# Kernel optimization log

Measured on AMD Instinct MI355X. Metric: run time of the kernel, lower is better.

The kernel has to match this reference:

```python
import jax, jax.numpy as jnp
import numpy as np

PS = 32
D = 256


def setup_inputs() -> dict:
    key = jax.random.key(0)
    ks = jax.random.split(key, 9)
    B, L = 32, 32768
    s_in = 1.0 / np.sqrt(PS)
    s_d = 1.0 / np.sqrt(D)
    return {
        "x": jax.random.normal(ks[0], (B, L), dtype=jnp.float32),
        "W_proj": jax.random.normal(ks[1], (PS, D), dtype=jnp.float32) * s_in,
        "b_proj": jnp.zeros((D,), jnp.float32),
        "W_qkv": jax.random.normal(ks[2], (D, 3 * D), dtype=jnp.float32) * s_d,
        "b_qkv": jnp.zeros((3 * D,), jnp.float32),
        "W_out": jax.random.normal(ks[3], (D, D), dtype=jnp.float32) * s_d,
        "b_out": jnp.zeros((D,), jnp.float32),
        "W_head": jax.random.normal(ks[4], (D, PS), dtype=jnp.float32) * s_d,
        "b_head": jnp.zeros((PS,), jnp.float32),
    }


def reference(x, W_proj, b_proj, W_qkv, b_qkv, W_out, b_out, W_head, b_head):
    B, L = x.shape
    T = L // PS
    # InstanceNorm over full series (torch .std is unbiased -> ddof=1)
    mean = jnp.mean(x, axis=-1, keepdims=True)
    std = jnp.std(x, axis=-1, keepdims=True, ddof=1) + 1e-5
    x_norm = (x - mean) / std
    patches = x_norm.reshape(B, T, PS)
    # Patch embedding
    h = patches @ W_proj + b_proj  # [B, T, D]
    # Single-head causal self-attention (explicit scores, as in source)
    qkv = h @ W_qkv + b_qkv
    q, k, v = jnp.split(qkv, 3, axis=-1)
    scale = 1.0 / jnp.sqrt(jnp.asarray(D, dtype=h.dtype))
    attn = jnp.einsum("btd,bsd->bts", q, k) * scale  # [B, T, T]
    causal = jnp.tril(jnp.ones((T, T), dtype=bool))
    attn = jnp.where(causal, attn, -jnp.inf)
    attn = jax.nn.softmax(attn, axis=-1)
    out = jnp.einsum("bts,bsd->btd", attn, v)
    out = out @ W_out + b_out
    # Prediction head + next-patch MSE loss
    pred = out @ W_head + b_head  # [B, T, PS]
    loss = jnp.mean((pred[:, :-1] - patches[:, 1:]) ** 2)
    return loss
```

## Files before the change

### kernel.cpp

```cpp
#include <hip/hip_runtime.h>
#include <math.h>

#define B_SZ 32
#define L_SZ 32768
#define T_SZ 1024
#define PS_SZ 32
#define D_SZ 256
#define SM_M 10.0f

typedef float f32x4 __attribute__((ext_vector_type(4)));
typedef short s16x8 __attribute__((ext_vector_type(8)));
typedef unsigned short u16x8 __attribute__((ext_vector_type(8)));
typedef unsigned short u16x4 __attribute__((ext_vector_type(4)));

__device__ __forceinline__ unsigned short f2bf(float f) {
  union { float f; unsigned int u; } v; v.f = f;
  unsigned int r = v.u + 0x7FFFu + ((v.u >> 16) & 1u);
  return (unsigned short)(r >> 16);
}

__device__ __forceinline__ void g2l16(const unsigned short* g, unsigned short* l) {
  __builtin_amdgcn_global_load_lds(
      (const __attribute__((address_space(1))) unsigned int*)g,
      (__attribute__((address_space(3))) unsigned int*)l, 16, 0, 0);
}

__global__ __launch_bounds__(256) void prep_kernel(const float* __restrict__ x,
                                                   float* __restrict__ sget,
                                                   const float* __restrict__ Wp,
                                                   const float* __restrict__ bp,
                                                   const float* __restrict__ Wq,
                                                   const float* __restrict__ bq,
                                                   const float* __restrict__ Wo,
                                                   const float* __restrict__ bo,
                                                   const float* __restrict__ Wh,
                                                   const float* __restrict__ bh,
                                                   float* __restrict__ Wcb,
                                                   unsigned short* __restrict__ WqT,
                                                   unsigned short* __restrict__ WfT,
                                                   float* __restrict__ bfp) {
  if (blockIdx.x < 256) {
    const int b = blockIdx.x >> 3;
    const float* p = x + (size_t)b * L_SZ + (size_t)(blockIdx.x & 7) * 4096;
    float s = 0.f, ss = 0.f;
#pragma unroll
    for (int i = 0; i < 4; ++i) {
      float4 f = ((const float4*)p)[threadIdx.x + i * 256];
      s += f.x + f.y + f.z + f.w;
      ss += f.x * f.x + f.y * f.y + f.z * f.z + f.w * f.w;
    }
#pragma unroll
    for (int off = 32; off >= 1; off >>= 1) {
      s += __shfl_down(s, off);
      ss += __shfl_down(ss, off);
    }
    __shared__ float rs[4], rss[4];
    const int wid = threadIdx.x >> 6, lane = threadIdx.x & 63;
    if (lane == 0) { rs[wid] = s; rss[wid] = ss; }
    __syncthreads();
    if (threadIdx.x == 0) {
      atomicAdd(&sget[b * 2],     rs[0] + rs[1] + rs[2] + rs[3]);
      atomicAdd(&sget[b * 2 + 1], rss[0] + rss[1] + rss[2] + rss[3]);
    }
  } else {
    int idx = (blockIdx.x - 256) * 256 + threadIdx.x;
    if (idx < 33 * 768) {
      int p = idx / 768, j = idx % 768;
      const float* arow = (p < 32) ? (Wp + p * 256) : bp;
      float acc = (p < 32) ? 0.f : bq[j];
      for (int d = 0; d < 256; ++d) acc += arow[d] * Wq[d * 768 + j];
      if (p < 32) WqT[j * 32 + p] = f2bf(acc);
      else Wcb[j] = acc;
    } else {
      int k = idx - 33 * 768;
      if (k < 8192) {
        int p = k >> 8, d = k & 255;
        float acc = 0.f;
        for (int e = 0; e < 256; ++e) acc += Wo[d * 256 + e] * Wh[e * 32 + p];
        WfT[p * 256 + d] = f2bf(acc);
      } else if (k < 8224) {
        int p = k - 8192;
        float acc = bh[p];
        for (int e = 0; e < 256; ++e) acc += bo[e] * Wh[e * 32 + p];
        bfp[p] = acc;
      }
    }
  }
}

__global__ __launch_bounds__(256) void gemm_qkv_mfma(const float* __restrict__ x,
                                                     const float* __restrict__ sget,
                                                     const unsigned short* __restrict__ WqT,
                                                     const float* __restrict__ biasq,
                                                     unsigned short* __restrict__ Qb,
                                                     unsigned short* __restrict__ Kb,
                                                     unsigned short* __restrict__ Vtt) {
  __shared__ unsigned short T4[4][8448];
  const int tid = threadIdx.x;
  const int w = tid >> 6, lane = tid & 63;
  const int lo = lane & 15, quad = lane >> 4;
  unsigned short* Tw = T4[w];
  const int mbase = blockIdx.x * 128 + w * 32;
  const int b = mbase >> 10;
  const float S = sget[b * 2], SS = sget[b * 2 + 1];
  const float mean = S * (1.f / (float)L_SZ);
  const float var = (SS - S * mean) * (1.f / (float)(L_SZ - 1));
  const float inv = 1.f / (sqrtf(var) + 1e-5f);
  s16x8 af0, af1;
  {
    float4 a = *(const float4*)&x[(size_t)(mbase + lo) * 32 + quad * 8];
    float4 c = *(const float4*)&x[(size_t)(mbase + lo) * 32 + quad * 8 + 4];
    af0[0] = (short)f2bf((a.x - mean) * inv); af0[1] = (short)f2bf((a.y - mean) * inv);
    af0[2] = (short)f2bf((a.z - mean) * inv); af0[3] = (short)f2bf((a.w - mean) * inv);
    af0[4] = (short)f2bf((c.x - mean) * inv); af0[5] = (short)f2bf((c.y - mean) * inv);
    af0[6] = (short)f2bf((c.z - mean) * inv); af0[7] = (short)f2bf((c.w - mean) * inv);
    float4 d = *(const float4*)&x[(size_t)(mbase + 16 + lo) * 32 + quad * 8];
    float4 e = *(const float4*)&x[(size_t)(mbase + 16 + lo) * 32 + quad * 8 + 4];
    af1[0] = (short)f2bf((d.x - mean) * inv); af1[1] = (short)f2bf((d.y - mean) * inv);
    af1[2] = (short)f2bf((d.z - mean) * inv); af1[3] = (short)f2bf((d.w - mean) * inv);
    af1[4] = (short)f2bf((e.x - mean) * inv); af1[5] = (short)f2bf((e.y - mean) * inv);
    af1[6] = (short)f2bf((e.z - mean) * inv); af1[7] = (short)f2bf((e.w - mean) * inv);
  }
#pragma unroll 4
  for (int nt = 0; nt < 16; ++nt) {
    s16x8 bf = *(const s16x8*)&WqT[(size_t)(nt * 16 + lo) * 32 + quad * 8];
    f32x4 c0 = {0.f, 0.f, 0.f, 0.f}, c1 = {0.f, 0.f, 0.f, 0.f};
    c0 = __builtin_amdgcn_mfma_f32_16x16x32_bf16(af0, bf, c0, 0, 0, 0);
    c1 = __builtin_amdgcn_mfma_f32_16x16x32_bf16(af1, bf, c1, 0, 0, 0);
    const int col = nt * 16 + lo;
    const float bi = biasq[col];
#pragma unroll
    for (int i = 0; i < 4; ++i) {
      Tw[(quad * 4 + i) * 264 + col]      = f2bf((c0[i] + bi) * 0.0625f);
      Tw[(16 + quad * 4 + i) * 264 + col] = f2bf((c1[i] + bi) * 0.0625f);
    }
  }
#pragma unroll
  for (int it = 0; it < 16; ++it) {
    const int gsub = it * 64 + lane;
    const int row = gsub >> 5, c16 = gsub & 31;
    *(u16x8*)&Qb[(size_t)(mbase + row) * 256 + c16 * 8] =
        *(const u16x8*)&Tw[row * 264 + c16 * 8];
  }
#pragma unroll 4
  for (int nt = 0; nt < 16; ++nt) {
    s16x8 bf = *(const s16x8*)&WqT[(size_t)(256 + nt * 16 + lo) * 32 + quad * 8];
    f32x4 c0 = {0.f, 0.f, 0.f, 0.f}, c1 = {0.f, 0.f, 0.f, 0.f};
    c0 = __builtin_amdgcn_mfma_f32_16x16x32_bf16(af0, bf, c0, 0, 0, 0);
    c1 = __builtin_amdgcn_mfma_f32_16x16x32_bf16(af1, bf, c1, 0, 0, 0);
    const int col = nt * 16 + lo;
    const float bi = biasq[256 + col];
#pragma unroll
    for (int i = 0; i < 4; ++i) {
      Tw[(quad * 4 + i) * 264 + col]      = f2bf(c0[i] + bi);
      Tw[(16 + quad * 4 + i) * 264 + col] = f2bf(c1[i] + bi);
    }
  }
#pragma unroll
  for (int it = 0; it < 16; ++it) {
    const int gsub = it * 64 + lane;
    const int row = gsub >> 5, c16 = gsub & 31;
    *(u16x8*)&Kb[(size_t)(mbase + row) * 256 + c16 * 8] =
        *(const u16x8*)&Tw[row * 264 + c16 * 8];
  }
#pragma unroll 4
  for (int nt2 = 0; nt2 < 16; ++nt2) {
    s16x8 aw = *(const s16x8*)&WqT[(size_t)(512 + nt2 * 16 + lo) * 32 + quad * 8];
    f32x4 c0 = {0.f, 0.f, 0.f, 0.f}, c1 = {0.f, 0.f, 0.f, 0.f};
    c0 = __builtin_amdgcn_mfma_f32_16x16x32_bf16(aw, af0, c0, 0, 0, 0);
    c1 = __builtin_amdgcn_mfma_f32_16x16x32_bf16(aw, af1, c1, 0, 0, 0);
#pragma unroll
    for (int i = 0; i < 4; ++i) {
      const int d = nt2 * 16 + quad * 4 + i;
      const float bv = biasq[512 + d];
      Tw[d * 32 + lo]      = f2bf(c0[i] + bv);
      Tw[d * 32 + 16 + lo] = f2bf(c1[i] + bv);
    }
  }
  {
    const int ktq = (mbase >> 5) & 31;
    const size_t vb = ((size_t)b * 32 + ktq) * 8192;
#pragma unroll
    for (int it = 0; it < 16; ++it) {
      const int gsub = it * 64 + lane;
      *(u16x8*)&Vtt[vb + gsub * 8] = *(const u16x8*)&Tw[gsub * 8];
    }
  }
}

__global__ __launch_bounds__(256) void attn_kernel(const unsigned short* __restrict__ Qb,
                                                   const unsigned short* __restrict__ Kb,
                                                   const unsigned short* __restrict__ Vtt,
                                                   const unsigned short* __restrict__ WfT,
                                                   const float* __restrict__ bfp,
                                                   const float* __restrict__ x,
                                                   const float* __restrict__ sget,
                                                   float* __restrict__ lsum) {
  __shared__ unsigned short SH[18944];
  const int g = blockIdx.x;
  const int j = g >> 3;
  const int b = (g & 7) * 4 + (j & 3);
  const int qt = 15 - (j >> 2);
  const int tid = threadIdx.x;
  const int w = tid >> 6, lane = tid & 63;
  const int lo = lane & 15, quad = lane >> 4;
  const int lo7 = lo & 7;
  const int qr0 = qt * 64 + w * 16;

  const size_t kbase = (size_t)b << 10;
  s16x8 qf[8];
  const size_t qrow = (kbase + qr0 + lo) * 256;
#pragma unroll
  for (int kc = 0; kc < 8; ++kc) qf[kc] = *(const s16x8*)&Qb[qrow + kc * 32 + quad * 8];

  f32x4 O[16];
#pragma unroll
  for (int nt = 0; nt < 16; ++nt) O[nt] = (f32x4){0.f, 0.f, 0.f, 0.f};
  f32x4 Ol = {0.f, 0.f, 0.f, 0.f};

  s16x8 ones;
#pragma unroll
  for (int jj = 0; jj < 8; ++jj) ones[jj] = (short)0x3F80;

  unsigned short* myp = &SH[16384 + w * 640];
  const int nk = 2 * (qt + 1);

  for (int kt = 0; kt < nk; ++kt) {
    const int k0 = kt * 32;
    __syncthreads();
#pragma unroll
    for (int it = 0; it < 4; ++it) {
      const int s = it * 256 + tid;
      const int key = s >> 5, c16p = s & 31;
      const int c16 = (c16p & 24) | ((c16p & 7) ^ (key & 7));
      g2l16(&Kb[((kbase + k0 + key) << 8) + (c16 << 3)], &SH[(it * 256 + w * 64) * 8]);
    }
    const size_t vb = ((size_t)b * 32 + kt) * 8192;
#pragma unroll
    for (int it = 0; it < 4; ++it) {
      const int s = it * 256 + tid;
      const int d = s >> 2, cp = s & 3;
      const int c = cp ^ ((d >> 1) & 3);
      g2l16(&Vtt[vb + ((d << 2) + c) * 8], &SH[8192 + (it * 256 + w * 64) * 8]);
    }
    __syncthreads();

    if (k0 <= qr0 + 15) {
      f32x4 s0 = {0.f, 0.f, 0.f, 0.f}, s1 = {0.f, 0.f, 0.f, 0.f};
#pragma unroll
      for (int kc = 0; kc < 8; ++kc) {
        const int c16 = kc * 4 + quad;
        const int cs = (c16 & 24) | ((c16 & 7) ^ lo7);
        s16x8 kf0 = *(const s16x8*)&SH[(lo * 32 + cs) * 8];
        s16x8 kf1 = *(const s16x8*)&SH[((16 + lo) * 32 + cs) * 8];
        s0 = __builtin_amdgcn_mfma_f32_16x16x32_bf16(qf[kc], kf0, s0, 0, 0, 0);
        s1 = __builtin_amdgcn_mfma_f32_16x16x32_bf16(qf[kc], kf1, s1, 0, 0, 0);
      }
      if (k0 + 31 > qr0) {
#pragma unroll
        for (int ii = 0; ii < 4; ++ii) {
          const int row = qr0 + quad * 4 + ii;
          if (k0 + lo > row) s0[ii] = -1e30f;
          if (k0 + 16 + lo > row) s1[ii] = -1e30f;
        }
      }
#pragma unroll
      for (int ii = 0; ii < 4; ++ii) {
        myp[(quad * 4 + ii) * 40 + lo]      = f2bf(__expf(s0[ii] - SM_M));
        myp[(quad * 4 + ii) * 40 + 16 + lo] = f2bf(__expf(s1[ii] - SM_M));
      }
      s16x8 pf = *(const s16x8*)&myp[lo * 40 + quad * 8];
      Ol = __builtin_amdgcn_mfma_f32_16x16x32_bf16(pf, ones, Ol, 0, 0, 0);
#pragma unroll
      for (int nt = 0; nt < 16; ++nt) {
        const int d = nt * 16 + lo;
        const int cp = quad ^ ((d >> 1) & 3);
        s16x8 vf = *(const s16x8*)&SH[8192 + ((d << 2) + cp) * 8];
        O[nt] = __builtin_amdgcn_mfma_f32_16x16x32_bf16(pf, vf, O[nt], 0, 0, 0);
      }
    }
  }
  __syncthreads();

  float inv4[4];
#pragma unroll
  for (int ii = 0; ii < 4; ++ii) inv4[ii] = 1.f / Ol[ii];
  unsigned short* OLw = &SH[w * 4224];
#pragma unroll
  for (int nt = 0; nt < 16; ++nt)
#pragma unroll
    for (int ii = 0; ii < 4; ++ii)
      OLw[(quad * 4 + ii) * 264 + nt * 16 + lo] = f2bf(O[nt][ii] * inv4[ii]);

  s16x8 af[8];
#pragma unroll
  for (int kc = 0; kc < 8; ++kc)
    af[kc] = *(const s16x8*)&OLw[lo * 264 + kc * 32 + quad * 8];

  const float S = sget[b * 2], SS = sget[b * 2 + 1];
  const float mean = S * (1.f / (float)L_SZ);
  const float var = (SS - S * mean) * (1.f / (float)(L_SZ - 1));
  const float invb = 1.f / (sqrtf(var) + 1e-5f);

  float lacc = 0.f;
#pragma unroll
  for (int nt = 0; nt < 2; ++nt) {
    f32x4 acc = {0.f, 0.f, 0.f, 0.f};
#pragma unroll
    for (int kc = 0; kc < 8; ++kc) {
      s16x8 bfr = *(const s16x8*)&WfT[(size_t)(nt * 16 + lo) * 256 + kc * 32 + quad * 8];
      acc = __builtin_amdgcn_mfma_f32_16x16x32_bf16(af[kc], bfr, acc, 0, 0, 0);
    }
    const float ba = bfp[nt * 16 + lo];
    const int p = nt * 16 + lo;
#pragma unroll
    for (int ii = 0; ii < 4; ++ii) {
      const int t = qr0 + quad * 4 + ii;
      if (t < 1023) {
        const float pr = acc[ii] + ba;
        const float tg = (x[(size_t)b * L_SZ + (t + 1) * 32 + p] - mean) * invb;
        const float d = pr - tg;
        lacc += d * d;
      }
    }
  }
#pragma unroll
  for (int off = 32; off >= 1; off >>= 1) lacc += __shfl_down(lacc, off);
  if (lane == 0) atomicAdd(lsum, lacc);
}

__global__ void finalize_kernel(const float* __restrict__ lsum, float* __restrict__ out) {
  out[0] = lsum[0] * (1.f / (float)(B_SZ * (T_SZ - 1) * PS_SZ));
}

extern "C" void kernel_launch(void* const* d_in, const int* in_sizes, int n_in,
                              void* d_out, int out_size, void* d_ws, size_t ws_size,
                              hipStream_t stream) {
  const float* x      = (const float*)d_in[0];
  const float* W_proj = (const float*)d_in[1];
  const float* b_proj = (const float*)d_in[2];
  const float* W_qkv  = (const float*)d_in[3];
  const float* b_qkv  = (const float*)d_in[4];
  const float* W_out  = (const float*)d_in[5];
  const float* b_out  = (const float*)d_in[6];
  const float* W_head = (const float*)d_in[7];
  const float* b_head = (const float*)d_in[8];
  float* out = (float*)d_out;

  char* ws = (char*)d_ws;
  unsigned short* Qb  = (unsigned short*)(ws);
  unsigned short* Kb  = (unsigned short*)(ws + (16ull << 20));
  unsigned short* Vtt = (unsigned short*)(ws + (32ull << 20));
  char* tail = ws + (48ull << 20);
  float*          Wcb  = (float*)(tail);
  unsigned short* WqT  = (unsigned short*)(tail + (4ull << 10));
  unsigned short* WfT  = (unsigned short*)(tail + (64ull << 10));
  float*          bfp  = (float*)(tail + (96ull << 10));
  float*          sget = (float*)(tail + (100ull << 10));
  float*          lsum = (float*)(tail + (100ull << 10) + 256);

  hipMemsetAsync(sget, 0, 512, stream);
  prep_kernel<<<388, 256, 0, stream>>>(x, sget, W_proj, b_proj, W_qkv, b_qkv,
                                       W_out, b_out, W_head, b_head,
                                       Wcb, WqT, WfT, bfp);
  gemm_qkv_mfma<<<256, 256, 0, stream>>>(x, sget, WqT, Wcb, Qb, Kb, Vtt);
  attn_kernel<<<512, 256, 0, stream>>>(Qb, Kb, Vtt, WfT, bfp, x, sget, lsum);
  finalize_kernel<<<1, 1, 0, stream>>>(lsum, out);
}
```

Baseline: 165.2 us.

## Fuse pipeline into one cooperative persistent kernel with grid syncs

Replaces the memset plus four-kernel chain with a single cooperative launch of 512 blocks that runs stats/weight folding, the QKV GEMM and the attention-plus-loss phases separated by grid.sync, and reduces the loss without atomics. Per-block partial statistics replace atomic accumulation, and the K/V load addressing is precomputed as incrementing pointers. A non-cooperative fallback path keeps three kernels and uses a counter-based last-block finalize. The change removes launch gaps and the memset, but runs the QKV phase with only two waves per block and pays grid-wide barriers.

```diff
diff --git a/kernel.cpp b/kernel.cpp
--- a/kernel.cpp
+++ b/kernel.cpp
@@ -1,5 +1,8 @@
 #include <hip/hip_runtime.h>
+#include <hip/hip_cooperative_groups.h>
 #include <math.h>
+
+namespace cg = cooperative_groups;
 
 #define B_SZ 32
 #define L_SZ 32768
@@ -11,7 +14,6 @@
 typedef float f32x4 __attribute__((ext_vector_type(4)));
 typedef short s16x8 __attribute__((ext_vector_type(8)));
 typedef unsigned short u16x8 __attribute__((ext_vector_type(8)));
-typedef unsigned short u16x4 __attribute__((ext_vector_type(4)));
 
 __device__ __forceinline__ unsigned short f2bf(float f) {
   union { float f; unsigned int u; } v; v.f = f;
@@ -25,84 +27,73 @@
       (__attribute__((address_space(3))) unsigned int*)l, 16, 0, 0);
 }
 
-__global__ __launch_bounds__(256) void prep_kernel(const float* __restrict__ x,
-                                                   float* __restrict__ sget,
-                                                   const float* __restrict__ Wp,
-                                                   const float* __restrict__ bp,
-                                                   const float* __restrict__ Wq,
-                                                   const float* __restrict__ bq,
-                                                   const float* __restrict__ Wo,
-                                                   const float* __restrict__ bo,
-                                                   const float* __restrict__ Wh,
-                                                   const float* __restrict__ bh,
-                                                   float* __restrict__ Wcb,
-                                                   unsigned short* __restrict__ WqT,
-                                                   unsigned short* __restrict__ WfT,
-                                                   float* __restrict__ bfp) {
-  if (blockIdx.x < 256) {
-    const int b = blockIdx.x >> 3;
-    const float* p = x + (size_t)b * L_SZ + (size_t)(blockIdx.x & 7) * 4096;
-    float s = 0.f, ss = 0.f;
-#pragma unroll
-    for (int i = 0; i < 4; ++i) {
-      float4 f = ((const float4*)p)[threadIdx.x + i * 256];
-      s += f.x + f.y + f.z + f.w;
-      ss += f.x * f.x + f.y * f.y + f.z * f.z + f.w * f.w;
-    }
-#pragma unroll
-    for (int off = 32; off >= 1; off >>= 1) {
-      s += __shfl_down(s, off);
-      ss += __shfl_down(ss, off);
-    }
-    __shared__ float rs[4], rss[4];
-    const int wid = threadIdx.x >> 6, lane = threadIdx.x & 63;
-    if (lane == 0) { rs[wid] = s; rss[wid] = ss; }
-    __syncthreads();
-    if (threadIdx.x == 0) {
-      atomicAdd(&sget[b * 2],     rs[0] + rs[1] + rs[2] + rs[3]);
-      atomicAdd(&sget[b * 2 + 1], rss[0] + rss[1] + rss[2] + rss[3]);
-    }
+
+__device__ __forceinline__ void phaseA_stats(const float* x, float* sgpart, int g, int tid,
+                                             int w, int lane, float* red) {
+  const int b = g >> 3;
+  const float* p = x + (size_t)b * L_SZ + (size_t)(g & 7) * 4096;
+  float s = 0.f, ss = 0.f;
+#pragma unroll
+  for (int i = 0; i < 4; ++i) {
+    float4 f = ((const float4*)p)[tid + i * 256];
+    s += f.x + f.y + f.z + f.w;
+    ss += f.x * f.x + f.y * f.y + f.z * f.z + f.w * f.w;
+  }
+#pragma unroll
+  for (int off = 32; off >= 1; off >>= 1) {
+    s += __shfl_down(s, off);
+    ss += __shfl_down(ss, off);
+  }
+  if (lane == 0) { red[w] = s; red[4 + w] = ss; }
+  __syncthreads();
+  if (tid == 0) {
+    sgpart[g * 2]     = red[0] + red[1] + red[2] + red[3];
+    sgpart[g * 2 + 1] = red[4] + red[5] + red[6] + red[7];
+  }
+  __syncthreads();
+}
+
+__device__ __forceinline__ void phaseA_folds(int idx, const float* Wp, const float* bp,
+                                             const float* Wq, const float* bq,
+                                             const float* Wo, const float* bo,
+                                             const float* Wh, const float* bh,
+                                             float* Wcb, unsigned short* WqT,
+                                             unsigned short* WfT, float* bfp) {
+  if (idx < 33 * 768) {
+    int p = idx / 768, j = idx % 768;
+    const float* arow = (p < 32) ? (Wp + p * 256) : bp;
+    float acc = (p < 32) ? 0.f : bq[j];
+    for (int d = 0; d < 256; ++d) acc += arow[d] * Wq[d * 768 + j];
+    if (p < 32) WqT[j * 32 + p] = f2bf(acc);
+    else Wcb[j] = acc;
   } else {
-    int idx = (blockIdx.x - 256) * 256 + threadIdx.x;
-    if (idx < 33 * 768) {
-      int p = idx / 768, j = idx % 768;
-      const float* arow = (p < 32) ? (Wp + p * 256) : bp;
-      float acc = (p < 32) ? 0.f : bq[j];
-      for (int d = 0; d < 256; ++d) acc += arow[d] * Wq[d * 768 + j];
-      if (p < 32) WqT[j * 32 + p] = f2bf(acc);
-      else Wcb[j] = acc;
-    } else {
-      int k = idx - 33 * 768;
-      if (k < 8192) {
-        int p = k >> 8, d = k & 255;
-        float acc = 0.f;
-        for (int e = 0; e < 256; ++e) acc += Wo[d * 256 + e] * Wh[e * 32 + p];
-        WfT[p * 256 + d] = f2bf(acc);
-      } else if (k < 8224) {
-        int p = k - 8192;
-        float acc = bh[p];
-        for (int e = 0; e < 256; ++e) acc += bo[e] * Wh[e * 32 + p];
-        bfp[p] = acc;
-      }
-    }
-  }
-}
-
-__global__ __launch_bounds__(256) void gemm_qkv_mfma(const float* __restrict__ x,
-                                                     const float* __restrict__ sget,
-                                                     const unsigned short* __restrict__ WqT,
-                                                     const float* __restrict__ biasq,
-                                                     unsigned short* __restrict__ Qb,
-                                                     unsigned short* __restrict__ Kb,
-                                                     unsigned short* __restrict__ Vtt) {
-  __shared__ unsigned short T4[4][8448];
-  const int tid = threadIdx.x;
-  const int w = tid >> 6, lane = tid & 63;
-  const int lo = lane & 15, quad = lane >> 4;
-  unsigned short* Tw = T4[w];
-  const int mbase = blockIdx.x * 128 + w * 32;
+    int k = idx - 33 * 768;
+    if (k < 8192) {
+      int p = k >> 8, d = k & 255;
+      float acc = 0.f;
+      for (int e = 0; e < 256; ++e) acc += Wo[d * 256 + e] * Wh[e * 32 + p];
+      WfT[p * 256 + d] = f2bf(acc);
+    } else if (k < 8224) {
+      int p = k - 8192;
+      float acc = bh[p];
+      for (int e = 0; e < 256; ++e) acc += bo[e] * Wh[e * 32 + p];
+      bfp[p] = acc;
+    }
+  }
+}
+
+__device__ __forceinline__ void qkv_wave(const float* x, const float* sgpart,
+                                         const unsigned short* WqT, const float* Wcb,
+                                         unsigned short* Qb, unsigned short* Kb,
+                                         unsigned short* Vtt, unsigned short* Tw,
+                                         int mbase, int lane, int lo, int quad) {
   const int b = mbase >> 10;
-  const float S = sget[b * 2], SS = sget[b * 2 + 1];
+  float S = 0.f, SS = 0.f;
+#pragma unroll
+  for (int i = 0; i < 8; ++i) {
+    S += sgpart[(b * 8 + i) * 2];
+    SS += sgpart[(b * 8 + i) * 2 + 1];
+  }
   const float mean = S * (1.f / (float)L_SZ);
   const float var = (SS - S * mean) * (1.f / (float)(L_SZ - 1));
   const float inv = 1.f / (sqrtf(var) + 1e-5f);
@@ -128,7 +119,7 @@
     c0 = __builtin_amdgcn_mfma_f32_16x16x32_bf16(af0, bf, c0, 0, 0, 0);
     c1 = __builtin_amdgcn_mfma_f32_16x16x32_bf16(af1, bf, c1, 0, 0, 0);
     const int col = nt * 16 + lo;
-    const float bi = biasq[col];
+    const float bi = Wcb[col];
 #pragma unroll
     for (int i = 0; i < 4; ++i) {
       Tw[(quad * 4 + i) * 264 + col]      = f2bf((c0[i] + bi) * 0.0625f);
@@ -149,7 +140,7 @@
     c0 = __builtin_amdgcn_mfma_f32_16x16x32_bf16(af0, bf, c0, 0, 0, 0);
     c1 = __builtin_amdgcn_mfma_f32_16x16x32_bf16(af1, bf, c1, 0, 0, 0);
     const int col = nt * 16 + lo;
-    const float bi = biasq[256 + col];
+    const float bi = Wcb[256 + col];
 #pragma unroll
     for (int i = 0; i < 4; ++i) {
       Tw[(quad * 4 + i) * 264 + col]      = f2bf(c0[i] + bi);
@@ -172,7 +163,7 @@
 #pragma unroll
     for (int i = 0; i < 4; ++i) {
       const int d = nt2 * 16 + quad * 4 + i;
-      const float bv = biasq[512 + d];
+      const float bv = Wcb[512 + d];
       Tw[d * 32 + lo]      = f2bf(c0[i] + bv);
       Tw[d * 32 + 16 + lo] = f2bf(c1[i] + bv);
     }
@@ -188,26 +179,16 @@
   }
 }
 
-__global__ __launch_bounds__(256) void attn_kernel(const unsigned short* __restrict__ Qb,
-                                                   const unsigned short* __restrict__ Kb,
-                                                   const unsigned short* __restrict__ Vtt,
-                                                   const unsigned short* __restrict__ WfT,
-                                                   const float* __restrict__ bfp,
-                                                   const float* __restrict__ x,
-                                                   const float* __restrict__ sget,
-                                                   float* __restrict__ lsum) {
-  __shared__ unsigned short SH[18944];
-  const int g = blockIdx.x;
-  const int j = g >> 3;
-  const int b = (g & 7) * 4 + (j & 3);
-  const int qt = 15 - (j >> 2);
-  const int tid = threadIdx.x;
-  const int w = tid >> 6, lane = tid & 63;
-  const int lo = lane & 15, quad = lane >> 4;
-  const int lo7 = lo & 7;
+__device__ __forceinline__ float attn_tile(const unsigned short* Qb,
+                                           const unsigned short* Kb,
+                                           const unsigned short* Vtt,
+                                           const unsigned short* WfT, const float* bfp,
+                                           const float* x, const float* sgpart,
+                                           unsigned short* SMEM, int b, int qt,
+                                           int tid, int w, int lane, int lo, int quad) {
   const int qr0 = qt * 64 + w * 16;
-
   const size_t kbase = (size_t)b << 10;
+
   s16x8 qf[8];
   const size_t qrow = (kbase + qr0 + lo) * 256;
 #pragma unroll
@@ -217,32 +198,32 @@
 #pragma unroll
   for (int nt = 0; nt < 16; ++nt) O[nt] = (f32x4){0.f, 0.f, 0.f, 0.f};
   f32x4 Ol = {0.f, 0.f, 0.f, 0.f};
-
   s16x8 ones;
 #pragma unroll
   for (int jj = 0; jj < 8; ++jj) ones[jj] = (short)0x3F80;
 
-  unsigned short* myp = &SH[16384 + w * 640];
+  const int c16p = tid & 31;
+  const int keyr = tid >> 5;
+  const int c16s = (c16p & 24) | ((c16p & 7) ^ keyr);
+  const unsigned short* kgp = Kb + (kbase << 8) + keyr * 256 + c16s * 8;
+  const int dql = tid >> 2;
+  const int cpq = (tid & 3) ^ ((tid >> 3) & 3);
+  const unsigned short* vgp = Vtt + (size_t)b * 262144 + dql * 32 + cpq * 8;
+
+  unsigned short* myp = &SMEM[16384 + w * 640];
+  const int lo7 = lo & 7;
   const int nk = 2 * (qt + 1);
 
   for (int kt = 0; kt < nk; ++kt) {
     const int k0 = kt * 32;
     __syncthreads();
 #pragma unroll
-    for (int it = 0; it < 4; ++it) {
-      const int s = it * 256 + tid;
-      const int key = s >> 5, c16p = s & 31;
-      const int c16 = (c16p & 24) | ((c16p & 7) ^ (key & 7));
-      g2l16(&Kb[((kbase + k0 + key) << 8) + (c16 << 3)], &SH[(it * 256 + w * 64) * 8]);
-    }
-    const size_t vb = ((size_t)b * 32 + kt) * 8192;
-#pragma unroll
-    for (int it = 0; it < 4; ++it) {
-      const int s = it * 256 + tid;
-      const int d = s >> 2, cp = s & 3;
-      const int c = cp ^ ((d >> 1) & 3);
-      g2l16(&Vtt[vb + ((d << 2) + c) * 8], &SH[8192 + (it * 256 + w * 64) * 8]);
-    }
+    for (int it = 0; it < 4; ++it)
+      g2l16(kgp + it * 2048, &SMEM[(it * 256 + w * 64) * 8]);
+#pragma unroll
+    for (int it = 0; it < 4; ++it)
+      g2l16(vgp + it * 2048, &SMEM[8192 + (it * 256 + w * 64) * 8]);
+    kgp += 8192; vgp += 8192;
     __syncthreads();
 
     if (k0 <= qr0 + 15) {
@@ -251,8 +232,8 @@
       for (int kc = 0; kc < 8; ++kc) {
         const int c16 = kc * 4 + quad;
         const int cs = (c16 & 24) | ((c16 & 7) ^ lo7);
-        s16x8 kf0 = *(const s16x8*)&SH[(lo * 32 + cs) * 8];
-        s16x8 kf1 = *(const s16x8*)&SH[((16 + lo) * 32 + cs) * 8];
+        s16x8 kf0 = *(const s16x8*)&SMEM[(lo * 32 + cs) * 8];
+        s16x8 kf1 = *(const s16x8*)&SMEM[((16 + lo) * 32 + cs) * 8];
         s0 = __builtin_amdgcn_mfma_f32_16x16x32_bf16(qf[kc], kf0, s0, 0, 0, 0);
         s1 = __builtin_amdgcn_mfma_f32_16x16x32_bf16(qf[kc], kf1, s1, 0, 0, 0);
       }
@@ -275,7 +256,7 @@
       for (int nt = 0; nt < 16; ++nt) {
         const int d = nt * 16 + lo;
         const int cp = quad ^ ((d >> 1) & 3);
-        s16x8 vf = *(const s16x8*)&SH[8192 + ((d << 2) + cp) * 8];
+        s16x8 vf = *(const s16x8*)&SMEM[8192 + ((d << 2) + cp) * 8];
         O[nt] = __builtin_amdgcn_mfma_f32_16x16x32_bf16(pf, vf, O[nt], 0, 0, 0);
       }
     }
@@ -285,7 +266,7 @@
   float inv4[4];
 #pragma unroll
   for (int ii = 0; ii < 4; ++ii) inv4[ii] = 1.f / Ol[ii];
-  unsigned short* OLw = &SH[w * 4224];
+  unsigned short* OLw = &SMEM[w * 4224];
 #pragma unroll
   for (int nt = 0; nt < 16; ++nt)
 #pragma unroll
@@ -297,7 +278,12 @@
   for (int kc = 0; kc < 8; ++kc)
     af[kc] = *(const s16x8*)&OLw[lo * 264 + kc * 32 + quad * 8];
 
-  const float S = sget[b * 2], SS = sget[b * 2 + 1];
+  float S = 0.f, SS = 0.f;
+#pragma unroll
+  for (int i = 0; i < 8; ++i) {
+    S += sgpart[(b * 8 + i) * 2];
+    SS += sgpart[(b * 8 + i) * 2 + 1];
+  }
   const float mean = S * (1.f / (float)L_SZ);
   const float var = (SS - S * mean) * (1.f / (float)(L_SZ - 1));
   const float invb = 1.f / (sqrtf(var) + 1e-5f);
@@ -326,11 +312,145 @@
   }
 #pragma unroll
   for (int off = 32; off >= 1; off >>= 1) lacc += __shfl_down(lacc, off);
-  if (lane == 0) atomicAdd(lsum, lacc);
-}
-
-__global__ void finalize_kernel(const float* __restrict__ lsum, float* __restrict__ out) {
-  out[0] = lsum[0] * (1.f / (float)(B_SZ * (T_SZ - 1) * PS_SZ));
+  float* redf = (float*)&SMEM[17024];
+  if (lane == 0) redf[w] = lacc;
+  __syncthreads();
+  return redf[0] + redf[1] + redf[2] + redf[3];
+}
+
+__global__ __launch_bounds__(256, 2) void mono_kernel(const float* __restrict__ x,
+                                                      const float* __restrict__ Wp,
+                                                      const float* __restrict__ bp,
+                                                      const float* __restrict__ Wq,
+                                                      const float* __restrict__ bq,
+                                                      const float* __restrict__ Wo,
+                                                      const float* __restrict__ bo,
+                                                      const float* __restrict__ Wh,
+                                                      const float* __restrict__ bh,
+                                                      char* __restrict__ ws,
+                                                      float* __restrict__ out) {
+  __shared__ unsigned short SMEM[18944];
+
+  unsigned short* Qb  = (unsigned short*)ws;
+  unsigned short* Kb  = (unsigned short*)(ws + (16ull << 20));
+  unsigned short* Vtt = (unsigned short*)(ws + (32ull << 20));
+  char* tail = ws + (48ull << 20);
+  float*          Wcb    = (float*)tail;
+  unsigned short* WqT    = (unsigned short*)(tail + 4096);
+  unsigned short* WfT    = (unsigned short*)(tail + 65536);
+  float*          bfp    = (float*)(tail + 98304);
+  float*          sgpart = (float*)(tail + 102400);
+  float*          lossb  = (float*)(tail + 104448);
+
+  const int g = blockIdx.x;
+  const int tid = threadIdx.x;
+  const int w = tid >> 6, lane = tid & 63;
+  const int lo = lane & 15, quad = lane >> 4;
+  cg::grid_group grid = cg::this_grid();
+
+  if (g < 256) {
+    phaseA_stats(x, sgpart, g, tid, w, lane, (float*)SMEM);
+  } else if (g < 388) {
+    phaseA_folds((g - 256) * 256 + tid, Wp, bp, Wq, bq, Wo, bo, Wh, bh, Wcb, WqT, WfT, bfp);
+  }
+  grid.sync();
+
+  if (w < 2)
+    qkv_wave(x, sgpart, WqT, Wcb, Qb, Kb, Vtt, &SMEM[w * 8448], g * 64 + w * 32, lane, lo, quad);
+  grid.sync();
+
+  {
+    const int p_ = g & 255, copy = g >> 8;
+    const int b = (p_ & 15) + copy * 16;
+    const int qtv = p_ >> 4;
+    const int qt = copy ? (15 - qtv) : qtv;
+    float bl = attn_tile(Qb, Kb, Vtt, WfT, bfp, x, sgpart, SMEM, b, qt, tid, w, lane, lo, quad);
+    if (tid == 0) lossb[g] = bl;
+  }
+  grid.sync();
+
+  if (g == 0 && tid < 64) {
+    float acc = 0.f;
+#pragma unroll
+    for (int i = 0; i < 8; ++i) acc += lossb[tid * 8 + i];
+#pragma unroll
+    for (int off = 32; off >= 1; off >>= 1) acc += __shfl_down(acc, off);
+    if (tid == 0) out[0] = acc * (1.f / (float)(B_SZ * (T_SZ - 1) * PS_SZ));
+  }
+}
+
+__global__ __launch_bounds__(256) void prep2_kernel(const float* __restrict__ x,
+                                                    float* __restrict__ sgpart,
+                                                    const float* __restrict__ Wp,
+                                                    const float* __restrict__ bp,
+                                                    const float* __restrict__ Wq,
+                                                    const float* __restrict__ bq,
+                                                    const float* __restrict__ Wo,
+                                                    const float* __restrict__ bo,
+                                                    const float* __restrict__ Wh,
+                                                    const float* __restrict__ bh,
+                                                    float* __restrict__ Wcb,
+                                                    unsigned short* __restrict__ WqT,
+                                                    unsigned short* __restrict__ WfT,
+                                                    float* __restrict__ bfp,
+                                                    float* __restrict__ lsum,
+                                                    unsigned int* __restrict__ counter) {
+  __shared__ float red[8];
+  const int g = blockIdx.x, tid = threadIdx.x;
+  const int w = tid >> 6, lane = tid & 63;
+  if (g < 256) {
+    phaseA_stats(x, sgpart, g, tid, w, lane, red);
+  } else if (g < 388) {
+    phaseA_folds((g - 256) * 256 + tid, Wp, bp, Wq, bq, Wo, bo, Wh, bh, Wcb, WqT, WfT, bfp);
+  } else if (tid == 0) {
+    lsum[0] = 0.f;
+    counter[0] = 0u;
+  }
+}
+
+__global__ __launch_bounds__(256) void qkv_kernel(const float* __restrict__ x,
+                                                  const float* __restrict__ sgpart,
+                                                  const unsigned short* __restrict__ WqT,
+                                                  const float* __restrict__ Wcb,
+                                                  unsigned short* __restrict__ Qb,
+                                                  unsigned short* __restrict__ Kb,
+                                                  unsigned short* __restrict__ Vtt) {
+  __shared__ unsigned short T4[4][8448];
+  const int tid = threadIdx.x;
+  const int w = tid >> 6, lane = tid & 63;
+  const int lo = lane & 15, quad = lane >> 4;
+  qkv_wave(x, sgpart, WqT, Wcb, Qb, Kb, Vtt, T4[w], blockIdx.x * 128 + w * 32, lane, lo, quad);
+}
+
+__global__ __launch_bounds__(256) void attn2_kernel(const unsigned short* __restrict__ Qb,
+                                                    const unsigned short* __restrict__ Kb,
+                                                    const unsigned short* __restrict__ Vtt,
+                                                    const unsigned short* __restrict__ WfT,
+                                                    const float* __restrict__ bfp,
+                                                    const float* __restrict__ x,
+                                                    const float* __restrict__ sgpart,
+                                                    float* __restrict__ lsum,
+                                                    unsigned int* __restrict__ counter,
+                                                    float* __restrict__ out) {
+  __shared__ unsigned short SMEM[18944];
+  const int g = blockIdx.x;
+  const int j = g >> 3;
+  const int b = (g & 7) * 4 + (j & 3);
+  const int qt = 15 - (j >> 2);
+  const int tid = threadIdx.x;
+  const int w = tid >> 6, lane = tid & 63;
+  const int lo = lane & 15, quad = lane >> 4;
+
+  float bl = attn_tile(Qb, Kb, Vtt, WfT, bfp, x, sgpart, SMEM, b, qt, tid, w, lane, lo, quad);
+  if (tid == 0) {
+    atomicAdd(lsum, bl);
+    __threadfence();
+    unsigned int prev = atomicAdd(counter, 1u);
+    if (prev == 511u) {
+      float total = atomicAdd(lsum, 0.0f);
+      out[0] = total * (1.f / (float)(B_SZ * (T_SZ - 1) * PS_SZ));
+    }
+  }
 }
 
 extern "C" void kernel_launch(void* const* d_in, const int* in_sizes, int n_in,
@@ -346,24 +466,37 @@
   const float* W_head = (const float*)d_in[7];
   const float* b_head = (const float*)d_in[8];
   float* out = (float*)d_out;
-
   char* ws = (char*)d_ws;
-  unsigned short* Qb  = (unsigned short*)(ws);
-  unsigned short* Kb  = (unsigned short*)(ws + (16ull << 20));
-  unsigned short* Vtt = (unsigned short*)(ws + (32ull << 20));
+
   char* tail = ws + (48ull << 20);
-  float*          Wcb  = (float*)(tail);
-  unsigned short* WqT  = (unsigned short*)(tail + (4ull << 10));
-  unsigned short* WfT  = (unsigned short*)(tail + (64ull << 10));
-  float*          bfp  = (float*)(tail + (96ull << 10));
-  float*          sget = (float*)(tail + (100ull << 10));
-  float*          lsum = (float*)(tail + (100ull << 10) + 256);
-
-  hipMemsetAsync(sget, 0, 512, stream);
-  prep_kernel<<<388, 256, 0, stream>>>(x, sget, W_proj, b_proj, W_qkv, b_qkv,
-                                       W_out, b_out, W_head, b_head,
-                                       Wcb, WqT, WfT, bfp);
-  gemm_qkv_mfma<<<256, 256, 0, stream>>>(x, sget, WqT, Wcb, Qb, Kb, Vtt);
-  attn_kernel<<<512, 256, 0, stream>>>(Qb, Kb, Vtt, WfT, bfp, x, sget, lsum);
-  finalize_kernel<<<1, 1, 0, stream>>>(lsum, out);
-}
+  unsigned short* Qb     = (unsigned short*)ws;
+  unsigned short* Kb     = (unsigned short*)(ws + (16ull << 20));
+  unsigned short* Vtt    = (unsigned short*)(ws + (32ull << 20));
+  float*          Wcb    = (float*)tail;
+  unsigned short* WqT    = (unsigned short*)(tail + 4096);
+  unsigned short* WfT    = (unsigned short*)(tail + 65536);
+  float*          bfp    = (float*)(tail + 98304);
+  float*          sgpart = (float*)(tail + 102400);
+  float*          lsum   = (float*)(tail + 106496);
+  unsigned int*   counter = (unsigned int*)(tail + 106752);
+
+  int maxb = 0;
+  hipError_t oe = hipOccupancyMaxActiveBlocksPerMultiprocessor(&maxb, mono_kernel, 256, 0);
+  bool coop_ok = (oe == hipSuccess) && (maxb >= 2);
+
+  if (coop_ok) {
+    void* args[] = {(void*)&x, (void*)&W_proj, (void*)&b_proj, (void*)&W_qkv, (void*)&b_qkv,
+                    (void*)&W_out, (void*)&b_out, (void*)&W_head, (void*)&b_head,
+                    (void*)&ws, (void*)&out};
+    hipError_t le = hipLaunchCooperativeKernel((const void*)mono_kernel, dim3(512), dim3(256),
+                                               args, 0, stream);
+    if (le == hipSuccess) return;
+    (void)hipGetLastError();
+  }
+
+  prep2_kernel<<<389, 256, 0, stream>>>(x, sgpart, W_proj, b_proj, W_qkv, b_qkv,
+                                        W_out, b_out, W_head, b_head,
+                                        Wcb, WqT, WfT, bfp, lsum, counter);
+  qkv_kernel<<<256, 256, 0, stream>>>(x, sgpart, WqT, Wcb, Qb, Kb, Vtt);
+  attn2_kernel<<<512, 256, 0, stream>>>(Qb, Kb, Vtt, WfT, bfp, x, sgpart, lsum, counter, out);
+}
```

After: 168.4 us. Within noise of the previous version (+1.9%).

## Double-buffer K/V tiles in attention and drop memset and finalize launches

Applied to the files above, without the earlier changes.

The attention kernel now double-buffers its K and V tiles in LDS, issuing the next tile's global-to-LDS loads before computing on the current one, so load latency overlaps with MFMA work. The per-tile barrier pair becomes a single barrier, and load addresses are precomputed and advanced by pointer increments. Row statistics are written as per-block partial sums instead of atomics, which removes the hipMemsetAsync. The finalize kernel is replaced by a last-block-done counter inside the attention kernel. This doubles LDS use per block, which may lower occupancy, and relies on a threadfence plus atomic-counter pattern to produce the final output.

```diff
diff --git a/kernel.cpp b/kernel.cpp
--- a/kernel.cpp
+++ b/kernel.cpp
@@ -11,7 +11,6 @@
 typedef float f32x4 __attribute__((ext_vector_type(4)));
 typedef short s16x8 __attribute__((ext_vector_type(8)));
 typedef unsigned short u16x8 __attribute__((ext_vector_type(8)));
-typedef unsigned short u16x4 __attribute__((ext_vector_type(4)));
 
 __device__ __forceinline__ unsigned short f2bf(float f) {
   union { float f; unsigned int u; } v; v.f = f;
@@ -26,7 +25,7 @@
 }
 
 __global__ __launch_bounds__(256) void prep_kernel(const float* __restrict__ x,
-                                                   float* __restrict__ sget,
+                                                   float* __restrict__ sgpart,
                                                    const float* __restrict__ Wp,
                                                    const float* __restrict__ bp,
                                                    const float* __restrict__ Wq,
@@ -38,14 +37,19 @@
                                                    float* __restrict__ Wcb,
                                                    unsigned short* __restrict__ WqT,
                                                    unsigned short* __restrict__ WfT,
-                                                   float* __restrict__ bfp) {
-  if (blockIdx.x < 256) {
-    const int b = blockIdx.x >> 3;
-    const float* p = x + (size_t)b * L_SZ + (size_t)(blockIdx.x & 7) * 4096;
+                                                   float* __restrict__ bfp,
+                                                   unsigned int* __restrict__ total,
+                                                   float* __restrict__ lsum) {
+  __shared__ float red[8];
+  const int g = blockIdx.x, tid = threadIdx.x;
+  const int w = tid >> 6, lane = tid & 63;
+  if (g < 256) {
+    const int b = g >> 3;
+    const float* p = x + (size_t)b * L_SZ + (size_t)(g & 7) * 4096;
     float s = 0.f, ss = 0.f;
 #pragma unroll
     for (int i = 0; i < 4; ++i) {
-      float4 f = ((const float4*)p)[threadIdx.x + i * 256];
+      float4 f = ((const float4*)p)[tid + i * 256];
       s += f.x + f.y + f.z + f.w;
       ss += f.x * f.x + f.y * f.y + f.z * f.z + f.w * f.w;
     }
@@ -54,16 +58,14 @@
       s += __shfl_down(s, off);
       ss += __shfl_down(ss, off);
     }
-    __shared__ float rs[4], rss[4];
-    const int wid = threadIdx.x >> 6, lane = threadIdx.x & 63;
-    if (lane == 0) { rs[wid] = s; rss[wid] = ss; }
+    if (lane == 0) { red[w] = s; red[4 + w] = ss; }
     __syncthreads();
-    if (threadIdx.x == 0) {
-      atomicAdd(&sget[b * 2],     rs[0] + rs[1] + rs[2] + rs[3]);
-      atomicAdd(&sget[b * 2 + 1], rss[0] + rss[1] + rss[2] + rss[3]);
-    }
-  } else {
-    int idx = (blockIdx.x - 256) * 256 + threadIdx.x;
+    if (tid == 0) {
+      sgpart[g * 2]     = red[0] + red[1] + red[2] + red[3];
+      sgpart[g * 2 + 1] = red[4] + red[5] + red[6] + red[7];
+    }
+  } else if (g < 388) {
+    int idx = (g - 256) * 256 + tid;
     if (idx < 33 * 768) {
       int p = idx / 768, j = idx % 768;
       const float* arow = (p < 32) ? (Wp + p * 256) : bp;
@@ -85,16 +87,18 @@
         bfp[p] = acc;
       }
     }
-  }
-}
-
-__global__ __launch_bounds__(256) void gemm_qkv_mfma(const float* __restrict__ x,
-                                                     const float* __restrict__ sget,
-                                                     const unsigned short* __restrict__ WqT,
-                                                     const float* __restrict__ biasq,
-                                                     unsigned short* __restrict__ Qb,
-                                                     unsigned short* __restrict__ Kb,
-                                                     unsigned short* __restrict__ Vtt) {
+  } else {
+    if (tid == 0) { total[0] = 0u; lsum[0] = 0.f; }
+  }
+}
+
+__global__ __launch_bounds__(256) void qkv_kernel(const float* __restrict__ x,
+                                                  const float* __restrict__ sgpart,
+                                                  const unsigned short* __restrict__ WqT,
+                                                  const float* __restrict__ Wcb,
+                                                  unsigned short* __restrict__ Qb,
+                                                  unsigned short* __restrict__ Kb,
+                                                  unsigned short* __restrict__ Vtt) {
   __shared__ unsigned short T4[4][8448];
   const int tid = threadIdx.x;
   const int w = tid >> 6, lane = tid & 63;
@@ -102,7 +106,12 @@
   unsigned short* Tw = T4[w];
   const int mbase = blockIdx.x * 128 + w * 32;
   const int b = mbase >> 10;
-  const float S = sget[b * 2], SS = sget[b * 2 + 1];
+  float S = 0.f, SS = 0.f;
+#pragma unroll
+  for (int i = 0; i < 8; ++i) {
+    S += sgpart[(b * 8 + i) * 2];
+    SS += sgpart[(b * 8 + i) * 2 + 1];
+  }
   const float mean = S * (1.f / (float)L_SZ);
   const float var = (SS - S * mean) * (1.f / (float)(L_SZ - 1));
   const float inv = 1.f / (sqrtf(var) + 1e-5f);
@@ -128,7 +137,7 @@
     c0 = __builtin_amdgcn_mfma_f32_16x16x32_bf16(af0, bf, c0, 0, 0, 0);
     c1 = __builtin_amdgcn_mfma_f32_16x16x32_bf16(af1, bf, c1, 0, 0, 0);
     const int col = nt * 16 + lo;
-    const float bi = biasq[col];
+    const float bi = Wcb[col];
 #pragma unroll
     for (int i = 0; i < 4; ++i) {
       Tw[(quad * 4 + i) * 264 + col]      = f2bf((c0[i] + bi) * 0.0625f);
@@ -149,7 +158,7 @@
     c0 = __builtin_amdgcn_mfma_f32_16x16x32_bf16(af0, bf, c0, 0, 0, 0);
     c1 = __builtin_amdgcn_mfma_f32_16x16x32_bf16(af1, bf, c1, 0, 0, 0);
     const int col = nt * 16 + lo;
-    const float bi = biasq[256 + col];
+    const float bi = Wcb[256 + col];
 #pragma unroll
     for (int i = 0; i < 4; ++i) {
       Tw[(quad * 4 + i) * 264 + col]      = f2bf(c0[i] + bi);
@@ -172,7 +181,7 @@
 #pragma unroll
     for (int i = 0; i < 4; ++i) {
       const int d = nt2 * 16 + quad * 4 + i;
-      const float bv = biasq[512 + d];
+      const float bv = Wcb[512 + d];
       Tw[d * 32 + lo]      = f2bf(c0[i] + bv);
       Tw[d * 32 + 16 + lo] = f2bf(c1[i] + bv);
     }
@@ -194,9 +203,11 @@
                                                    const unsigned short* __restrict__ WfT,
                                                    const float* __restrict__ bfp,
                                                    const float* __restrict__ x,
-                                                   const float* __restrict__ sget,
-                                                   float* __restrict__ lsum) {
-  __shared__ unsigned short SH[18944];
+                                                   const float* __restrict__ sgpart,
+                                                   float* __restrict__ lsum,
+                                                   unsigned int* __restrict__ total,
+                                                   float* __restrict__ out) {
+  __shared__ unsigned short SMEM[35328];
   const int g = blockIdx.x;
   const int j = g >> 3;
   const int b = (g & 7) * 4 + (j & 3);
@@ -204,10 +215,10 @@
   const int tid = threadIdx.x;
   const int w = tid >> 6, lane = tid & 63;
   const int lo = lane & 15, quad = lane >> 4;
-  const int lo7 = lo & 7;
+
   const int qr0 = qt * 64 + w * 16;
-
   const size_t kbase = (size_t)b << 10;
+
   s16x8 qf[8];
   const size_t qrow = (kbase + qr0 + lo) * 256;
 #pragma unroll
@@ -217,33 +228,42 @@
 #pragma unroll
   for (int nt = 0; nt < 16; ++nt) O[nt] = (f32x4){0.f, 0.f, 0.f, 0.f};
   f32x4 Ol = {0.f, 0.f, 0.f, 0.f};
-
   s16x8 ones;
 #pragma unroll
   for (int jj = 0; jj < 8; ++jj) ones[jj] = (short)0x3F80;
 
-  unsigned short* myp = &SH[16384 + w * 640];
+  const int c16p = tid & 31;
+  const int keyr = tid >> 5;
+  const int c16s = (c16p & 24) | ((c16p & 7) ^ keyr);
+  const unsigned short* kgp = Kb + (kbase << 8) + keyr * 256 + c16s * 8;
+  const int dql = tid >> 2;
+  const int cpq = (tid & 3) ^ ((tid >> 3) & 3);
+  const unsigned short* vgp = Vtt + (size_t)b * 262144 + dql * 32 + cpq * 8;
+  const int ldst = (w * 64) * 8;
+
+  unsigned short* myp = &SMEM[32768 + w * 640];
+  const int lo7 = lo & 7;
   const int nk = 2 * (qt + 1);
+
+#pragma unroll
+  for (int it = 0; it < 4; ++it) g2l16(kgp + it * 2048, &SMEM[it * 2048 + ldst]);
+#pragma unroll
+  for (int it = 0; it < 4; ++it) g2l16(vgp + it * 2048, &SMEM[8192 + it * 2048 + ldst]);
+  kgp += 8192; vgp += 8192;
 
   for (int kt = 0; kt < nk; ++kt) {
     const int k0 = kt * 32;
     __syncthreads();
-#pragma unroll
-    for (int it = 0; it < 4; ++it) {
-      const int s = it * 256 + tid;
-      const int key = s >> 5, c16p = s & 31;
-      const int c16 = (c16p & 24) | ((c16p & 7) ^ (key & 7));
-      g2l16(&Kb[((kbase + k0 + key) << 8) + (c16 << 3)], &SH[(it * 256 + w * 64) * 8]);
-    }
-    const size_t vb = ((size_t)b * 32 + kt) * 8192;
-#pragma unroll
-    for (int it = 0; it < 4; ++it) {
-      const int s = it * 256 + tid;
-      const int d = s >> 2, cp = s & 3;
-      const int c = cp ^ ((d >> 1) & 3);
-      g2l16(&Vtt[vb + ((d << 2) + c) * 8], &SH[8192 + (it * 256 + w * 64) * 8]);
-    }
-    __syncthreads();
+    const int cur = (kt & 1) << 14;
+    if (kt + 1 < nk) {
+      const int nxt = ((kt + 1) & 1) << 14;
+#pragma unroll
+      for (int it = 0; it < 4; ++it) g2l16(kgp + it * 2048, &SMEM[nxt + it * 2048 + ldst]);
+#pragma unroll
+      for (int it = 0; it < 4; ++it)
+        g2l16(vgp + it * 2048, &SMEM[nxt + 8192 + it * 2048 + ldst]);
+      kgp += 8192; vgp += 8192;
+    }
 
     if (k0 <= qr0 + 15) {
       f32x4 s0 = {0.f, 0.f, 0.f, 0.f}, s1 = {0.f, 0.f, 0.f, 0.f};
@@ -251,8 +271,8 @@
       for (int kc = 0; kc < 8; ++kc) {
         const int c16 = kc * 4 + quad;
         const int cs = (c16 & 24) | ((c16 & 7) ^ lo7);
-        s16x8 kf0 = *(const s16x8*)&SH[(lo * 32 + cs) * 8];
-        s16x8 kf1 = *(const s16x8*)&SH[((16 + lo) * 32 + cs) * 8];
+        s16x8 kf0 = *(const s16x8*)&SMEM[cur + (lo * 32 + cs) * 8];
+        s16x8 kf1 = *(const s16x8*)&SMEM[cur + ((16 + lo) * 32 + cs) * 8];
         s0 = __builtin_amdgcn_mfma_f32_16x16x32_bf16(qf[kc], kf0, s0, 0, 0, 0);
         s1 = __builtin_amdgcn_mfma_f32_16x16x32_bf16(qf[kc], kf1, s1, 0, 0, 0);
       }
@@ -275,7 +295,7 @@
       for (int nt = 0; nt < 16; ++nt) {
         const int d = nt * 16 + lo;
         const int cp = quad ^ ((d >> 1) & 3);
-        s16x8 vf = *(const s16x8*)&SH[8192 + ((d << 2) + cp) * 8];
+        s16x8 vf = *(const s16x8*)&SMEM[cur + 8192 + ((d << 2) + cp) * 8];
         O[nt] = __builtin_amdgcn_mfma_f32_16x16x32_bf16(pf, vf, O[nt], 0, 0, 0);
       }
     }
@@ -285,7 +305,7 @@
   float inv4[4];
 #pragma unroll
   for (int ii = 0; ii < 4; ++ii) inv4[ii] = 1.f / Ol[ii];
-  unsigned short* OLw = &SH[w * 4224];
+  unsigned short* OLw = &SMEM[w * 4224];
 #pragma unroll
   for (int nt = 0; nt < 16; ++nt)
 #pragma unroll
@@ -297,7 +317,12 @@
   for (int kc = 0; kc < 8; ++kc)
     af[kc] = *(const s16x8*)&OLw[lo * 264 + kc * 32 + quad * 8];
 
-  const float S = sget[b * 2], SS = sget[b * 2 + 1];
+  float S = 0.f, SS = 0.f;
+#pragma unroll
+  for (int i = 0; i < 8; ++i) {
+    S += sgpart[(b * 8 + i) * 2];
+    SS += sgpart[(b * 8 + i) * 2 + 1];
+  }
   const float mean = S * (1.f / (float)L_SZ);
   const float var = (SS - S * mean) * (1.f / (float)(L_SZ - 1));
   const float invb = 1.f / (sqrtf(var) + 1e-5f);
@@ -326,11 +351,22 @@
   }
 #pragma unroll
   for (int off = 32; off >= 1; off >>= 1) lacc += __shfl_down(lacc, off);
-  if (lane == 0) atomicAdd(lsum, lacc);
-}
-
-__global__ void finalize_kernel(const float* __restrict__ lsum, float* __restrict__ out) {
-  out[0] = lsum[0] * (1.f / (float)(B_SZ * (T_SZ - 1) * PS_SZ));
+  float* redf = (float*)&SMEM[35000];
+  unsigned int* flag = (unsigned int*)&SMEM[35100];
+  if (lane == 0) redf[w] = lacc;
+  __syncthreads();
+
+  if (tid == 0) {
+    atomicAdd(lsum, redf[0] + redf[1] + redf[2] + redf[3]);
+    __threadfence();
+    unsigned int prev = atomicAdd(total, 1u);
+    flag[0] = (prev == 511u) ? 1u : 0u;
+  }
+  __syncthreads();
+  if (flag[0] && tid == 0) {
+    float tot = atomicAdd(lsum, 0.0f);
+    out[0] = tot * (1.f / (float)(B_SZ * (T_SZ - 1) * PS_SZ));
+  }
 }
 
 extern "C" void kernel_launch(void* const* d_in, const int* in_sizes, int n_in,
@@ -346,24 +382,23 @@
   const float* W_head = (const float*)d_in[7];
   const float* b_head = (const float*)d_in[8];
   float* out = (float*)d_out;
-
   char* ws = (char*)d_ws;
-  unsigned short* Qb  = (unsigned short*)(ws);
-  unsigned short* Kb  = (unsigned short*)(ws + (16ull << 20));
-  unsigned short* Vtt = (unsigned short*)(ws + (32ull << 20));
+
+  unsigned short* Qb     = (unsigned short*)ws;
+  unsigned short* Kb     = (unsigned short*)(ws + (16ull << 20));
+  unsigned short* Vtt    = (unsigned short*)(ws + (32ull << 20));
   char* tail = ws + (48ull << 20);
-  float*          Wcb  = (float*)(tail);
-  unsigned short* WqT  = (unsigned short*)(tail + (4ull << 10));
-  unsigned short* WfT  = (unsigned short*)(tail + (64ull << 10));
-  float*          bfp  = (float*)(tail + (96ull << 10));
-  float*          sget = (float*)(tail + (100ull << 10));
-  float*          lsum = (float*)(tail + (100ull << 10) + 256);
-
-  hipMemsetAsync(sget, 0, 512, stream);
-  prep_kernel<<<388, 256, 0, stream>>>(x, sget, W_proj, b_proj, W_qkv, b_qkv,
+  float*          Wcb    = (float*)tail;
+  unsigned short* WqT    = (unsigned short*)(tail + 4096);
+  unsigned short* WfT    = (unsigned short*)(tail + 65536);
+  float*          bfp    = (float*)(tail + 98304);
+  float*          sgpart = (float*)(tail + 102400);
+  unsigned int*   total  = (unsigned int*)(tail + 106496);
+  float*          lsum   = (float*)(tail + 106496 + 64);
+
+  prep_kernel<<<389, 256, 0, stream>>>(x, sgpart, W_proj, b_proj, W_qkv, b_qkv,
                                        W_out, b_out, W_head, b_head,
-                                       Wcb, WqT, WfT, bfp);
-  gemm_qkv_mfma<<<256, 256, 0, stream>>>(x, sget, WqT, Wcb, Qb, Kb, Vtt);
-  attn_kernel<<<512, 256, 0, stream>>>(Qb, Kb, Vtt, WfT, bfp, x, sget, lsum);
-  finalize_kernel<<<1, 1, 0, stream>>>(lsum, out);
-}
+                                       Wcb, WqT, WfT, bfp, total, lsum);
+  qkv_kernel<<<256, 256, 0, stream>>>(x, sgpart, WqT, Wcb, Qb, Kb, Vtt);
+  attn_kernel<<<512, 256, 0, stream>>>(Qb, Kb, Vtt, WfT, bfp, x, sgpart, lsum, total, out);
+}
```

After: 163.2 us, median of 2. Within noise of the previous version (-1.2%).
